# Performance work log

Hardware: AMD Instinct MI355X
Metric: run time of the kernel (lower is better)

The kernel has to match this reference:

```python
import jax, jax.numpy as jnp
import numpy as np
import math

B, C, D, H, W = 1, 64, 16, 16, 16
HEADS = 4
HD = C // HEADS  # head_dim = 16


def conv3d(x, w, b, pad):
    # x: [B,C,D,H,W], w: [O,I,kd,kh,kw], pad: (pd,ph,pw)
    y = jax.lax.conv_general_dilated(
        x, w, window_strides=(1, 1, 1),
        padding=[(p, p) for p in pad],
        dimension_numbers=('NCDHW', 'OIDHW', 'NCDHW'))
    return y + b[None, :, None, None, None]


def setup_inputs() -> dict:
    key = jax.random.key(0)
    ks = jax.random.split(key, 10)
    s = 0.02
    return {
        'x': jax.random.normal(ks[0], (B, C, D, H, W), jnp.float32),
        'gamma': jax.random.normal(ks[1], (1,), jnp.float32),
        'w_sp': jax.random.normal(ks[2], (C, C, 1, 3, 3), jnp.float32) * s,
        'b_sp': jax.random.normal(ks[3], (C,), jnp.float32) * s,
        'w_spec': jax.random.normal(ks[4], (C, C, 3, 1, 1), jnp.float32) * s,
        'b_spec': jax.random.normal(ks[5], (C,), jnp.float32) * s,
        'w_qkv': jax.random.normal(ks[6], (3 * C, C, 1, 1, 1), jnp.float32) * s,
        'b_qkv': jax.random.normal(ks[7], (3 * C,), jnp.float32) * s,
        'w_proj': jax.random.normal(ks[8], (C, C, 1, 1, 1), jnp.float32) * s,
        'b_proj': jax.random.normal(ks[9], (C,), jnp.float32) * s,
    }


def _decay_exponent(dtype):
    # Faithful to the torch permute quirk (requires H == W):
    # exponent[i,j,k,m,n,o] = |i-m| + |j-k| + |n-o|
    dd = jnp.abs(jnp.arange(D)[:, None] - jnp.arange(D)[None, :]).astype(dtype)  # [D,D]
    hh = jnp.abs(jnp.arange(H)[:, None] - jnp.arange(H)[None, :]).astype(dtype)  # [H,H]
    ww = jnp.abs(jnp.arange(W)[:, None] - jnp.arange(W)[None, :]).astype(dtype)  # [W,W]
    return (dd[:, None, None, :, None, None]      # i (axis0), m (axis3)
            + hh[None, :, :, None, None, None]    # j (axis1), k (axis2)
            + ww[None, None, None, None, :, :])   # n (axis4), o (axis5)


def _forward(x, gamma, w_sp, b_sp, w_spec, b_spec, w_qkv, b_qkv, w_proj, b_proj):
    x = conv3d(x, w_sp, b_sp, (0, 1, 1))
    x = conv3d(x, w_spec, b_spec, (1, 0, 0))
    qkv = conv3d(x, w_qkv, b_qkv, (0, 0, 0))
    q, k, v = jnp.split(qkv, 3, axis=1)
    rs = lambda t: t.reshape(B, HEADS, HD, D, H, W)
    q, k, v = rs(q), rs(k), rs(v)

    g = jax.nn.sigmoid(gamma[0])
    decay = g ** _decay_exponent(x.dtype)  # [D,H,W,D,W,W] (H==W)

    # attn[b,h,i,j,k,m,n,o]: (i,j,k)=query D,H,W ; (m,n,o)=key D,H,W
    attn = jnp.einsum('bhdijk,bhdmno->bhijkmno', q, k) / math.sqrt(HD)
    attn = jax.nn.softmax(attn * decay, axis=-1)  # softmax over key-W axis o only
    out = jnp.einsum('bhijkmno,bhdmno->bhdijk', attn, v)
    out = out.reshape(B, C, D, H, W)
    return conv3d(out, w_proj, b_proj, (0, 0, 0))


def reference(x, gamma, w_sp, b_sp, w_spec, b_spec, w_qkv, b_qkv, w_proj, b_proj):
    return _forward(x, gamma, w_sp, b_sp, w_spec, b_spec, w_qkv, b_qkv, w_proj, b_proj)
```

## Files before the change

kernel.cpp:

```cpp
#include <hip/hip_runtime.h>
#include <math.h>

#define CN   262144

typedef __attribute__((ext_vector_type(8))) short short8;
typedef __attribute__((ext_vector_type(4))) short short4v;
typedef __attribute__((ext_vector_type(4))) float float4v;

static __device__ __forceinline__ unsigned short f2bf(float f) {
    union { float f; unsigned u; } v; v.f = f;
    unsigned r = (v.u + 0x7FFFu + ((v.u >> 16) & 1u)) >> 16;
    return (unsigned short)r;
}

__global__ __launch_bounds__(512) void wfuse_kernel(
        const float* __restrict__ w_spec, const float* __restrict__ b_spec,
        const float* __restrict__ w_qkv, const float* __restrict__ b_qkv,
        unsigned short* __restrict__ wfb, float* __restrict__ bfv) {
    int idx = blockIdx.x * 512 + threadIdx.x;
    int oc = idx / 192;
    int r  = idx % 192;
    float s = 0.f;
    #pragma unroll 8
    for (int ci = 0; ci < 64; ++ci)
        s += w_qkv[oc * 64 + ci] * w_spec[ci * 192 + r];
    if (oc < 64) s *= 0.25f;
    wfb[oc * 192 + r] = f2bf(s);
    if (idx < 192) {
        float t = b_qkv[idx];
        for (int ci = 0; ci < 64; ++ci) t += w_qkv[idx * 64 + ci] * b_spec[ci];
        if (idx < 64) t *= 0.25f;
        bfv[idx] = t;
    }
}

__global__ __launch_bounds__(512) void conv_sp_kernel(
        const float* __restrict__ x, const float* __restrict__ w,
        const float* __restrict__ b, float* __restrict__ y) {
    __shared__ float ws[576];
    __shared__ float red[8][256];
    int co = blockIdx.x >> 4;
    int d  = blockIdx.x & 15;
    int tid = threadIdx.x;
    for (int idx = tid; idx < 576; idx += 512) ws[idx] = w[co * 576 + idx];
    __syncthreads();
    int og  = tid & 63;
    int grp = tid >> 6;
    int h = og >> 2, wq = og & 3;
    float ax = 0.f, ay = 0.f, az = 0.f, aw = 0.f;
    #pragma unroll 4
    for (int c2 = 0; c2 < 8; ++c2) {
        int ci = grp * 8 + c2;
        const float* row = x + ci * 4096 + d * 256;
        const float* wc  = ws + ci * 9;
        #pragma unroll
        for (int dh = 0; dh < 3; ++dh) {
            int hh = h + dh - 1;
            if (hh < 0 || hh > 15) continue;
            const float* r = row + hh * 16 + wq * 4;
            float4 q0 = *(const float4*)r;
            float lm = (wq > 0) ? r[-1] : 0.f;
            float rp = (wq < 3) ? r[4]  : 0.f;
            float wL = wc[dh * 3 + 0], wM = wc[dh * 3 + 1], wR = wc[dh * 3 + 2];
            ax += wL * lm   + wM * q0.x + wR * q0.y;
            ay += wL * q0.x + wM * q0.y + wR * q0.z;
            az += wL * q0.y + wM * q0.z + wR * q0.w;
            aw += wL * q0.z + wM * q0.w + wR * rp;
        }
    }
    float4 part = {ax, ay, az, aw};
    *(float4*)&red[grp][og * 4] = part;
    __syncthreads();
    if (tid < 256) {
        float s = b[co];
        #pragma unroll
        for (int g = 0; g < 8; ++g) s += red[g][tid];
        y[co * 4096 + d * 256 + tid] = s;
    }
}

#define BTP 196
__global__ __launch_bounds__(512, 2) void qkv_mfma_kernel(
        const float* __restrict__ y1, const unsigned short* __restrict__ wfb,
        const float* __restrict__ bfv,
        unsigned short* __restrict__ qb, unsigned short* __restrict__ kb,
        unsigned short* __restrict__ vtb) {
    __shared__ __align__(16) unsigned short Bt[64 * BTP];
    int bI  = blockIdx.x;
    int ocg = bI % 3;
    int pq  = (bI / 3) & 3;
    int d   = bI / 12;
    int tid = threadIdx.x;

    {
        int px  = tid & 63;
        int cig = tid >> 6;
        const float* yb = y1 + d * 256 + pq * 64 + px;
        #pragma unroll 2
        for (int cc = 0; cc < 8; ++cc) {
            int ci = cig * 8 + cc;
            const float* yc = yb + ci * 4096;
            #pragma unroll
            for (int t = 0; t < 3; ++t) {
                float v = 0.f;
                if (!((d == 0 && t == 0) || (d == 15 && t == 2)))
                    v = yc[(t - 1) * 256];
                Bt[px * BTP + ci * 3 + t] = f2bf(v);
            }
        }
    }

    int wv = tid >> 6, lane = tid & 63;
    int quad = lane >> 4, l15 = lane & 15;
    int Mt = wv >> 1;
    int nb = (wv & 1) * 2;

    short8 af[6];
    {
        const unsigned short* ab = wfb + (ocg * 64 + Mt * 16 + l15) * 192 + quad * 8;
        #pragma unroll
        for (int ks = 0; ks < 6; ++ks) af[ks] = *(const short8*)(ab + ks * 32);
    }
    float bias[4];
    #pragma unroll
    for (int r = 0; r < 4; ++r) bias[r] = bfv[ocg * 64 + Mt * 16 + quad * 4 + r];

    __syncthreads();

    float4v czero = {0.f, 0.f, 0.f, 0.f};
    float4v acc[2] = {czero, czero};
    #pragma unroll
    for (int nt = 0; nt < 2; ++nt) {
        const unsigned short* brow = Bt + ((nb + nt) * 16 + l15) * BTP + quad * 8;
        #pragma unroll
        for (int ks = 0; ks < 6; ++ks) {
            short4v lo = *(const short4v*)(brow + ks * 32);
            short4v hi = *(const short4v*)(brow + ks * 32 + 4);
            short8 bf8 = {lo[0], lo[1], lo[2], lo[3], hi[0], hi[1], hi[2], hi[3]};
            acc[nt] = __builtin_amdgcn_mfma_f32_16x16x32_bf16(af[ks], bf8, acc[nt], 0, 0, 0);
        }
    }

    #pragma unroll
    for (int nt = 0; nt < 2; ++nt) {
        int p = d * 256 + pq * 64 + (nb + nt) * 16 + l15;
        if (ocg == 2) {
            int h = (p >> 4) & 15, w0 = p & 15;
            int kap = 8 * (w0 >> 2) + 4 * (h & 1) + (w0 & 3);
            unsigned short* dst = vtb + ((Mt * 16 + d) * 8 + (h >> 1)) * 512
                                      + (quad * 4) * 32 + kap;
            #pragma unroll
            for (int r = 0; r < 4; ++r) dst[r * 32] = f2bf(acc[nt][r] + bias[r]);
        } else {
            unsigned short* dst = (ocg == 0 ? qb : kb) + Mt * 65536 + p * 16 + quad * 4;
            unsigned t0 = (unsigned)f2bf(acc[nt][0] + bias[0])
                        | ((unsigned)f2bf(acc[nt][1] + bias[1]) << 16);
            unsigned t1 = (unsigned)f2bf(acc[nt][2] + bias[2])
                        | ((unsigned)f2bf(acc[nt][3] + bias[3]) << 16);
            *(unsigned*)dst = t0;
            *(unsigned*)(dst + 2) = t1;
        }
    }
}

__global__ __launch_bounds__(512, 2) void attn_kernel(
        const unsigned short* __restrict__ qb, const unsigned short* __restrict__ kb,
        const unsigned short* __restrict__ vtb, const float* __restrict__ gamma,
        float* __restrict__ ao0, float* __restrict__ ao1,
        float* __restrict__ ao2, float* __restrict__ ao3) {
    __shared__ __align__(16) unsigned short ksh[4096];
    __shared__ __align__(16) unsigned short vsh[4096];
    __shared__ float gp[32];
    int tid = threadIdx.x;
    int bI = blockIdx.x;
    int head = bI >> 7;
    int mg   = (bI >> 5) & 3;
    int oct  = bI & 31;

    if (tid < 32) {
        float g = 1.f / (1.f + __expf(-gamma[0]));
        gp[tid] = __powf(g, (float)tid);
    }

    int wv = tid >> 6, lane = tid & 63;
    int quad = lane >> 4, l15 = lane & 15;
    int t = oct * 8 + wv;
    int i = t >> 4, j = t & 15;

    short8 zero8 = {0, 0, 0, 0, 0, 0, 0, 0};
    float4v czero = {0.f, 0.f, 0.f, 0.f};

    short8 qf = zero8;
    if (quad < 2)
        qf = *(const short8*)(qb + head * 65536 + (t * 16 + l15) * 16 + quad * 8);

    __syncthreads();
    float wd[4];
    #pragma unroll
    for (int r = 0; r < 4; ++r) wd[r] = gp[abs(l15 - (quad * 4 + r))];

    float4v O = czero;

    for (int mm = 0; mm < 4; ++mm) {
        int m = mg * 4 + mm;
        __syncthreads();
        ((float4*)ksh)[tid] = ((const float4*)(kb  + head * 65536 + m * 4096))[tid];
        ((float4*)vsh)[tid] = ((const float4*)(vtb + (head * 16 + m) * 4096))[tid];
        __syncthreads();

        int eim = abs(i - m);
        #pragma unroll
        for (int np = 0; np < 8; ++np) {
            short8 a2 = zero8;
            #pragma unroll
            for (int s = 0; s < 2; ++s) {
                int n = np * 2 + s;
                short8 a1 = zero8;
                if (quad < 2)
                    a1 = *(const short8*)(ksh + n * 256 + l15 * 16 + quad * 8);
                float4v d1 = __builtin_amdgcn_mfma_f32_16x16x32_bf16(a1, qf, czero, 0, 0, 0);
                float smn = gp[eim + abs(j - n)];
                float e0 = __expf(d1[0] * smn * wd[0]);
                float e1 = __expf(d1[1] * smn * wd[1]);
                float e2 = __expf(d1[2] * smn * wd[2]);
                float e3 = __expf(d1[3] * smn * wd[3]);
                float sm = e0 + e1 + e2 + e3;
                sm += __shfl_xor(sm, 16);
                sm += __shfl_xor(sm, 32);
                float inv = __builtin_amdgcn_rcpf(sm);
                a2[s * 4 + 0] = (short)f2bf(e0 * inv);
                a2[s * 4 + 1] = (short)f2bf(e1 * inv);
                a2[s * 4 + 2] = (short)f2bf(e2 * inv);
                a2[s * 4 + 3] = (short)f2bf(e3 * inv);
            }
            short8 b2 = *(const short8*)(vsh + np * 512 + l15 * 32 + quad * 8);
            O = __builtin_amdgcn_mfma_f32_16x16x32_bf16(a2, b2, O, 0, 0, 0);
        }
    }

    float* aop = (mg == 0) ? ao0 : ((mg == 1) ? ao1 : ((mg == 2) ? ao2 : ao3));
    float4 ov = {O[0], O[1], O[2], O[3]};
    *(float4*)(aop + (head * 16 + l15) * 4096 + t * 16 + quad * 4) = ov;
}

#define PTP 68
__global__ __launch_bounds__(256) void proj_mfma_kernel(
        const float* __restrict__ ao0, const float* __restrict__ ao1,
        const float* __restrict__ ao2, const float* __restrict__ ao3,
        const float* __restrict__ w, const float* __restrict__ b,
        float* __restrict__ out) {
    __shared__ __align__(16) unsigned short Bt[16 * PTP];
    int d   = blockIdx.x >> 4;
    int p16 = blockIdx.x & 15;
    int tid = threadIdx.x;

    {
        int px = tid & 15, cig = tid >> 4;
        int gbase = d * 256 + p16 * 16 + px;
        #pragma unroll
        for (int cc = 0; cc < 4; ++cc) {
            int ci = cig * 4 + cc;
            int ga = ci * 4096 + gbase;
            float v = ao0[ga] + ao1[ga] + ao2[ga] + ao3[ga];
            Bt[px * PTP + ci] = f2bf(v);
        }
    }
    __syncthreads();

    int wv = tid >> 6, lane = tid & 63;
    int quad = lane >> 4, l15 = lane & 15;
    float4v czero = {0.f, 0.f, 0.f, 0.f};
    float4v acc = czero;

    short8 af[2];
    const float* wsrc = w + (wv * 16 + l15) * 64 + quad * 8;
    #pragma unroll
    for (int ks = 0; ks < 2; ++ks) {
        float4 wa = *(const float4*)(wsrc + ks * 32);
        float4 wb = *(const float4*)(wsrc + ks * 32 + 4);
        short8 a8 = {(short)f2bf(wa.x), (short)f2bf(wa.y), (short)f2bf(wa.z),
                     (short)f2bf(wa.w), (short)f2bf(wb.x), (short)f2bf(wb.y),
                     (short)f2bf(wb.z), (short)f2bf(wb.w)};
        af[ks] = a8;
    }
    const unsigned short* brow = Bt + l15 * PTP + quad * 8;
    #pragma unroll
    for (int ks = 0; ks < 2; ++ks) {
        short4v lo = *(const short4v*)(brow + ks * 32);
        short4v hi = *(const short4v*)(brow + ks * 32 + 4);
        short8 bf8 = {lo[0], lo[1], lo[2], lo[3], hi[0], hi[1], hi[2], hi[3]};
        acc = __builtin_amdgcn_mfma_f32_16x16x32_bf16(af[ks], bf8, acc, 0, 0, 0);
    }

    int p = d * 256 + p16 * 16 + l15;
    #pragma unroll
    for (int r = 0; r < 4; ++r) {
        int oc = wv * 16 + quad * 4 + r;
        out[oc * 4096 + p] = acc[r] + b[oc];
    }
}

extern "C" void kernel_launch(void* const* d_in, const int* in_sizes, int n_in,
                              void* d_out, int out_size, void* d_ws, size_t ws_size,
                              hipStream_t stream) {
    const float* x      = (const float*)d_in[0];
    const float* gamma  = (const float*)d_in[1];
    const float* w_sp   = (const float*)d_in[2];
    const float* b_sp   = (const float*)d_in[3];
    const float* w_spec = (const float*)d_in[4];
    const float* b_spec = (const float*)d_in[5];
    const float* w_qkv  = (const float*)d_in[6];
    const float* b_qkv  = (const float*)d_in[7];
    const float* w_proj = (const float*)d_in[8];
    const float* b_proj = (const float*)d_in[9];
    float* out = (float*)d_out;

    float* ws = (float*)d_ws;
    float* y1  = ws;
    unsigned short* wfb = (unsigned short*)(ws + CN);
    float* bfv = ws + CN + 20480;
    unsigned short* qb  = (unsigned short*)(ws + 2 * CN);
    unsigned short* kb  = (unsigned short*)(ws + 2 * CN + CN / 2);
    unsigned short* vtb = (unsigned short*)(ws + 3 * CN);
    float* ao0 = y1;
    float* ao1 = ws + 3 * CN + CN / 2;
    float* ao2 = ws + 4 * CN + CN / 2;
    float* ao3 = ws + 5 * CN + CN / 2;

    wfuse_kernel    <<<  72, 512, 0, stream>>>(w_spec, b_spec, w_qkv, b_qkv, wfb, bfv);
    conv_sp_kernel  <<<1024, 512, 0, stream>>>(x, w_sp, b_sp, y1);
    qkv_mfma_kernel <<< 192, 512, 0, stream>>>(y1, wfb, bfv, qb, kb, vtb);
    attn_kernel     <<< 512, 512, 0, stream>>>(qb, kb, vtb, gamma, ao0, ao1, ao2, ao3);
    proj_mfma_kernel<<< 256, 256, 0, stream>>>(ao0, ao1, ao2, ao3, w_proj, b_proj, out);
}
```

Before: 142.9 us.

## Merge weight-fuse into spatial conv, halve qkv tiles, prefetch K/V in attention

```diff
diff --git a/kernel.cpp b/kernel.cpp
--- a/kernel.cpp
+++ b/kernel.cpp
@@ -13,30 +13,30 @@
     return (unsigned short)r;
 }
 
-__global__ __launch_bounds__(512) void wfuse_kernel(
+__global__ __launch_bounds__(512) void conv_sp_wfuse_kernel(
+        const float* __restrict__ x, const float* __restrict__ w,
+        const float* __restrict__ b, float* __restrict__ y,
         const float* __restrict__ w_spec, const float* __restrict__ b_spec,
         const float* __restrict__ w_qkv, const float* __restrict__ b_qkv,
         unsigned short* __restrict__ wfb, float* __restrict__ bfv) {
-    int idx = blockIdx.x * 512 + threadIdx.x;
-    int oc = idx / 192;
-    int r  = idx % 192;
-    float s = 0.f;
-    #pragma unroll 8
-    for (int ci = 0; ci < 64; ++ci)
-        s += w_qkv[oc * 64 + ci] * w_spec[ci * 192 + r];
-    if (oc < 64) s *= 0.25f;
-    wfb[oc * 192 + r] = f2bf(s);
-    if (idx < 192) {
-        float t = b_qkv[idx];
-        for (int ci = 0; ci < 64; ++ci) t += w_qkv[idx * 64 + ci] * b_spec[ci];
-        if (idx < 64) t *= 0.25f;
-        bfv[idx] = t;
-    }
-}
-
-__global__ __launch_bounds__(512) void conv_sp_kernel(
-        const float* __restrict__ x, const float* __restrict__ w,
-        const float* __restrict__ b, float* __restrict__ y) {
+    if (blockIdx.x >= 1024) {
+        int idx = (blockIdx.x - 1024) * 512 + threadIdx.x;
+        int oc = idx / 192;
+        int r  = idx % 192;
+        float s = 0.f;
+        #pragma unroll 8
+        for (int ci = 0; ci < 64; ++ci)
+            s += w_qkv[oc * 64 + ci] * w_spec[ci * 192 + r];
+        if (oc < 64) s *= 0.25f;
+        wfb[oc * 192 + r] = f2bf(s);
+        if (idx < 192) {
+            float t = b_qkv[idx];
+            for (int ci = 0; ci < 64; ++ci) t += w_qkv[idx * 64 + ci] * b_spec[ci];
+            if (idx < 64) t *= 0.25f;
+            bfv[idx] = t;
+        }
+        return;
+    }
     __shared__ float ws[576];
     __shared__ float red[8][256];
     int co = blockIdx.x >> 4;
@@ -85,20 +85,20 @@
         const float* __restrict__ bfv,
         unsigned short* __restrict__ qb, unsigned short* __restrict__ kb,
         unsigned short* __restrict__ vtb) {
-    __shared__ __align__(16) unsigned short Bt[64 * BTP];
+    __shared__ __align__(16) unsigned short Bt[32 * BTP];
     int bI  = blockIdx.x;
     int ocg = bI % 3;
-    int pq  = (bI / 3) & 3;
-    int d   = bI / 12;
+    int pq  = (bI / 3) & 7;
+    int d   = bI / 24;
     int tid = threadIdx.x;
 
     {
-        int px  = tid & 63;
-        int cig = tid >> 6;
-        const float* yb = y1 + d * 256 + pq * 64 + px;
-        #pragma unroll 2
-        for (int cc = 0; cc < 8; ++cc) {
-            int ci = cig * 8 + cc;
+        int px  = tid & 31;
+        int cig = tid >> 5;
+        const float* yb = y1 + d * 256 + pq * 32 + px;
+        #pragma unroll
+        for (int cc = 0; cc < 4; ++cc) {
+            int ci = cig * 4 + cc;
             const float* yc = yb + ci * 4096;
             #pragma unroll
             for (int t = 0; t < 3; ++t) {
@@ -113,7 +113,7 @@
     int wv = tid >> 6, lane = tid & 63;
     int quad = lane >> 4, l15 = lane & 15;
     int Mt = wv >> 1;
-    int nb = (wv & 1) * 2;
+    int nt = wv & 1;
 
     short8 af[6];
     {
@@ -128,35 +128,33 @@
     __syncthreads();
 
     float4v czero = {0.f, 0.f, 0.f, 0.f};
-    float4v acc[2] = {czero, czero};
-    #pragma unroll
-    for (int nt = 0; nt < 2; ++nt) {
-        const unsigned short* brow = Bt + ((nb + nt) * 16 + l15) * BTP + quad * 8;
+    float4v acc = czero;
+    {
+        const unsigned short* brow = Bt + (nt * 16 + l15) * BTP + quad * 8;
         #pragma unroll
         for (int ks = 0; ks < 6; ++ks) {
             short4v lo = *(const short4v*)(brow + ks * 32);
             short4v hi = *(const short4v*)(brow + ks * 32 + 4);
             short8 bf8 = {lo[0], lo[1], lo[2], lo[3], hi[0], hi[1], hi[2], hi[3]};
-            acc[nt] = __builtin_amdgcn_mfma_f32_16x16x32_bf16(af[ks], bf8, acc[nt], 0, 0, 0);
-        }
-    }
-
-    #pragma unroll
-    for (int nt = 0; nt < 2; ++nt) {
-        int p = d * 256 + pq * 64 + (nb + nt) * 16 + l15;
+            acc = __builtin_amdgcn_mfma_f32_16x16x32_bf16(af[ks], bf8, acc, 0, 0, 0);
+        }
+    }
+
+    {
+        int p = d * 256 + pq * 32 + nt * 16 + l15;
         if (ocg == 2) {
             int h = (p >> 4) & 15, w0 = p & 15;
             int kap = 8 * (w0 >> 2) + 4 * (h & 1) + (w0 & 3);
             unsigned short* dst = vtb + ((Mt * 16 + d) * 8 + (h >> 1)) * 512
                                       + (quad * 4) * 32 + kap;
             #pragma unroll
-            for (int r = 0; r < 4; ++r) dst[r * 32] = f2bf(acc[nt][r] + bias[r]);
+            for (int r = 0; r < 4; ++r) dst[r * 32] = f2bf(acc[r] + bias[r]);
         } else {
             unsigned short* dst = (ocg == 0 ? qb : kb) + Mt * 65536 + p * 16 + quad * 4;
-            unsigned t0 = (unsigned)f2bf(acc[nt][0] + bias[0])
-                        | ((unsigned)f2bf(acc[nt][1] + bias[1]) << 16);
-            unsigned t1 = (unsigned)f2bf(acc[nt][2] + bias[2])
-                        | ((unsigned)f2bf(acc[nt][3] + bias[3]) << 16);
+            unsigned t0 = (unsigned)f2bf(acc[0] + bias[0])
+                        | ((unsigned)f2bf(acc[1] + bias[1]) << 16);
+            unsigned t1 = (unsigned)f2bf(acc[2] + bias[2])
+                        | ((unsigned)f2bf(acc[3] + bias[3]) << 16);
             *(unsigned*)dst = t0;
             *(unsigned*)(dst + 2) = t1;
         }
@@ -194,24 +192,34 @@
     if (quad < 2)
         qf = *(const short8*)(qb + head * 65536 + (t * 16 + l15) * 16 + quad * 8);
 
+    const unsigned short* kbh = kb  + head * 65536 + mg * 4 * 4096;
+    const unsigned short* vbh = vtb + head * 65536 + mg * 4 * 4096;
+    float4 kpre = ((const float4*)kbh)[tid];
+    float4 vpre = ((const float4*)vbh)[tid];
+
     __syncthreads();
     float wd[4];
     #pragma unroll
-    for (int r = 0; r < 4; ++r) wd[r] = gp[abs(l15 - (quad * 4 + r))];
+    for (int r = 0; r < 4; ++r)
+        wd[r] = gp[abs(l15 - (quad * 4 + r))] * 1.4426950408889634f;
 
     float4v O = czero;
 
     for (int mm = 0; mm < 4; ++mm) {
         int m = mg * 4 + mm;
         __syncthreads();
-        ((float4*)ksh)[tid] = ((const float4*)(kb  + head * 65536 + m * 4096))[tid];
-        ((float4*)vsh)[tid] = ((const float4*)(vtb + (head * 16 + m) * 4096))[tid];
+        ((float4*)ksh)[tid] = kpre;
+        ((float4*)vsh)[tid] = vpre;
         __syncthreads();
+        if (mm < 3) {
+            kpre = ((const float4*)(kbh + (mm + 1) * 4096))[tid];
+            vpre = ((const float4*)(vbh + (mm + 1) * 4096))[tid];
+        }
 
         int eim = abs(i - m);
         #pragma unroll
         for (int np = 0; np < 8; ++np) {
-            short8 a2 = zero8;
+            union { unsigned u[4]; short8 s8; } a2u;
             #pragma unroll
             for (int s = 0; s < 2; ++s) {
                 int n = np * 2 + s;
@@ -220,21 +228,22 @@
                     a1 = *(const short8*)(ksh + n * 256 + l15 * 16 + quad * 8);
                 float4v d1 = __builtin_amdgcn_mfma_f32_16x16x32_bf16(a1, qf, czero, 0, 0, 0);
                 float smn = gp[eim + abs(j - n)];
-                float e0 = __expf(d1[0] * smn * wd[0]);
-                float e1 = __expf(d1[1] * smn * wd[1]);
-                float e2 = __expf(d1[2] * smn * wd[2]);
-                float e3 = __expf(d1[3] * smn * wd[3]);
+                float e0 = __builtin_amdgcn_exp2f(d1[0] * smn * wd[0]);
+                float e1 = __builtin_amdgcn_exp2f(d1[1] * smn * wd[1]);
+                float e2 = __builtin_amdgcn_exp2f(d1[2] * smn * wd[2]);
+                float e3 = __builtin_amdgcn_exp2f(d1[3] * smn * wd[3]);
                 float sm = e0 + e1 + e2 + e3;
                 sm += __shfl_xor(sm, 16);
                 sm += __shfl_xor(sm, 32);
                 float inv = __builtin_amdgcn_rcpf(sm);
-                a2[s * 4 + 0] = (short)f2bf(e0 * inv);
-                a2[s * 4 + 1] = (short)f2bf(e1 * inv);
-                a2[s * 4 + 2] = (short)f2bf(e2 * inv);
-                a2[s * 4 + 3] = (short)f2bf(e3 * inv);
+                union { float f; unsigned u; } p0, p1, p2, p3;
+                p0.f = e0 * inv; p1.f = e1 * inv;
+                p2.f = e2 * inv; p3.f = e3 * inv;
+                a2u.u[s * 2]     = ((p0.u + 0x8000u) >> 16) | ((p1.u + 0x8000u) & 0xFFFF0000u);
+                a2u.u[s * 2 + 1] = ((p2.u + 0x8000u) >> 16) | ((p3.u + 0x8000u) & 0xFFFF0000u);
             }
             short8 b2 = *(const short8*)(vsh + np * 512 + l15 * 32 + quad * 8);
-            O = __builtin_amdgcn_mfma_f32_16x16x32_bf16(a2, b2, O, 0, 0, 0);
+            O = __builtin_amdgcn_mfma_f32_16x16x32_bf16(a2u.s8, b2, O, 0, 0, 0);
         }
     }
 
@@ -327,9 +336,10 @@
     float* ao2 = ws + 4 * CN + CN / 2;
     float* ao3 = ws + 5 * CN + CN / 2;
 
-    wfuse_kernel    <<<  72, 512, 0, stream>>>(w_spec, b_spec, w_qkv, b_qkv, wfb, bfv);
-    conv_sp_kernel  <<<1024, 512, 0, stream>>>(x, w_sp, b_sp, y1);
-    qkv_mfma_kernel <<< 192, 512, 0, stream>>>(y1, wfb, bfv, qb, kb, vtb);
+    conv_sp_wfuse_kernel<<<1096, 512, 0, stream>>>(x, w_sp, b_sp, y1,
+                                                   w_spec, b_spec, w_qkv, b_qkv,
+                                                   wfb, bfv);
+    qkv_mfma_kernel <<< 384, 512, 0, stream>>>(y1, wfb, bfv, qb, kb, vtb);
     attn_kernel     <<< 512, 512, 0, stream>>>(qb, kb, vtb, gamma, ao0, ao1, ao2, ao3);
     proj_mfma_kernel<<< 256, 256, 0, stream>>>(ao0, ao1, ao2, ao3, w_proj, b_proj, out);
 }
```

Result: faster. 133.6 us (-6.5%).
